# Performance work log

Measured on AMD Instinct MI355X. Metric: run time of the kernel, lower is better.

Reference implementation:

```python
import jax, jax.numpy as jnp
import numpy as np

N, E, D = 50000, 800000, 128

def setup_inputs() -> dict:
    key = jax.random.key(0)
    ks = jax.random.split(key, 8)
    s = 0.02
    x = jax.random.normal(ks[0], (N, D), dtype=jnp.float32)
    edge_index = jax.random.randint(ks[1], (2, E), 0, N, dtype=jnp.int64)
    Wn = jax.random.normal(ks[2], (D, D), dtype=jnp.float32) * s
    bn = jax.random.normal(ks[3], (D,), dtype=jnp.float32) * s
    We = jax.random.normal(ks[4], (D, 2 * D), dtype=jnp.float32) * s
    be = jax.random.normal(ks[5], (D,), dtype=jnp.float32) * s
    Wu = jax.random.normal(ks[6], (D, 3 * D), dtype=jnp.float32) * s
    bu = jax.random.normal(ks[7], (D,), dtype=jnp.float32) * s
    return {"x": x, "edge_index": edge_index, "Wn": Wn, "bn": bn,
            "We": We, "be": be, "Wu": Wu, "bu": bu}

def reference(x, edge_index, Wn, bn, We, be, Wu, bu):
    n = x.shape[0]
    # 1. per-node linear transform (torch Linear: x @ W.T + b)
    node = x @ Wn.T + bn                                   # [N, D]
    src, dst = edge_index[0], edge_index[1]
    # 2. per-edge embedding from concatenated endpoint node embeddings
    edge_in = jnp.concatenate([node[src], node[dst]], axis=1)  # [E, 2D]
    edge_emb = edge_in @ We.T + be                          # [E, D]
    # 3. scatter-sum neighbor node embeddings and incident edge embeddings to src vertex
    nbr_sum = jax.ops.segment_sum(node[dst], src, num_segments=n)    # [N, D]
    edge_sum = jax.ops.segment_sum(edge_emb, src, num_segments=n)   # [N, D]
    pre_gelu = jnp.concatenate([node, nbr_sum, edge_sum], axis=1)    # [N, 3D]
    # 4-5. GELU (exact, matching torch nn.GELU default) + final linear
    out = jax.nn.gelu(pre_gelu, approximate=False) @ Wu.T + bu       # [N, D]
    return out
```

## Files before the change

### kernel.cpp

```cpp
#include <hip/hip_runtime.h>
#include <hip/hip_bf16.h>
#include <math.h>

typedef __attribute__((ext_vector_type(8))) short short8;
typedef __attribute__((ext_vector_type(4))) float f32x4;

#define CAP8 16
#define EPT  8

__device__ __forceinline__ float bf2f(unsigned short u) {
    union { unsigned int i; float f; } c; c.i = ((unsigned int)u) << 16; return c.f;
}
__device__ __forceinline__ unsigned short f2bf(float f) {
    __hip_bfloat16 h = __float2bfloat16(f);
    union { __hip_bfloat16 h; unsigned short u; } c; c.h = h; return c.u;
}
__device__ __forceinline__ float gelu_exact(float x) {
    return 0.5f * x * (1.0f + erff(x * 0.7071067811865475f));
}
__device__ __forceinline__ short8 ldcvt8(const float* p) {
    float4 f0 = *(const float4*)p;
    float4 f1 = *(const float4*)(p + 4);
    short8 a;
    a[0] = (short)f2bf(f0.x); a[1] = (short)f2bf(f0.y);
    a[2] = (short)f2bf(f0.z); a[3] = (short)f2bf(f0.w);
    a[4] = (short)f2bf(f1.x); a[5] = (short)f2bf(f1.y);
    a[6] = (short)f2bf(f1.z); a[7] = (short)f2bf(f1.w);
    return a;
}
__device__ __forceinline__ int swz(int row, int colbyte) {
    return row * 256 + (colbyte ^ ((row & 7) << 4));
}

__device__ __forceinline__ int detect_flag(const int* ei, int E) {
    int orv = 0;
    int lim = (E < 64) ? E : 64;
    for (int i = 0; i < lim; i++) orv |= ei[2 * i + 1];
    return (orv == 0) ? 1 : 0;
}
__device__ __forceinline__ int ld_src(const int* ei, int flag, int E, int e) {
    if (flag) { int2 p = *(const int2*)(ei + 2 * (size_t)e); return p.x; }
    return ei[e];
}
__device__ __forceinline__ int ld_dst(const int* ei, int flag, int E, int e) {
    if (flag) { int2 p = *(const int2*)(ei + 2 * (size_t)(E + e)); return p.x; }
    return ei[E + e];
}

__launch_bounds__(256)
__global__ void init_kernel(const float* __restrict__ Wn, const float* __restrict__ We,
                            const float* __restrict__ Wu,
                            unsigned short* __restrict__ Wnb, unsigned short* __restrict__ Web,
                            unsigned short* __restrict__ Wub,
                            int* __restrict__ cursor8, int N) {
    const int stride = gridDim.x * 256;
    const int t = blockIdx.x * 256 + threadIdx.x;
    for (int i = t; i < 8 * N; i += stride) cursor8[i] = 0;
    for (int i = t; i < 128 * 128; i += stride) Wnb[i] = f2bf(Wn[i]);
    for (int i = t; i < 128 * 256; i += stride) Web[i] = f2bf(We[i]);
    for (int i = t; i < 128 * 384; i += stride) Wub[i] = f2bf(Wu[i]);
}

__device__ __forceinline__ void gemm1_body(int bid,
                                           const float* __restrict__ x,
                                           const unsigned short* __restrict__ Wnb,
                                           const float* __restrict__ bias,
                                           unsigned short* __restrict__ node,
                                           unsigned short* __restrict__ Apre0,
                                           int N) {
    const int v0 = bid * 64;
    const int wave = threadIdx.x >> 6;
    const int lane = threadIdx.x & 63;
    const int m    = lane & 15;
    const int kq   = lane >> 4;

    short8 B[2][4];
#pragma unroll
    for (int ntl = 0; ntl < 2; ntl++) {
        const int j = (wave * 2 + ntl) * 16 + m;
#pragma unroll
        for (int kb = 0; kb < 4; kb++)
            B[ntl][kb] = *(const short8*)(Wnb + (size_t)j * 128 + kb * 32 + kq * 8);
    }

    f32x4 acc[4][2];
#pragma unroll
    for (int mt = 0; mt < 4; mt++)
#pragma unroll
        for (int ntl = 0; ntl < 2; ntl++) acc[mt][ntl] = (f32x4){0.f,0.f,0.f,0.f};

#pragma unroll
    for (int kb = 0; kb < 4; kb++) {
#pragma unroll
        for (int mt = 0; mt < 4; mt++) {
            const int row = v0 + mt * 16 + m;
            short8 a = (short8){0,0,0,0,0,0,0,0};
            if (row < N) a = ldcvt8(x + (size_t)row * 128 + kb * 32 + kq * 8);
#pragma unroll
            for (int ntl = 0; ntl < 2; ntl++)
                acc[mt][ntl] = __builtin_amdgcn_mfma_f32_16x16x32_bf16(a, B[ntl][kb], acc[mt][ntl], 0, 0, 0);
        }
    }

    const int ocol = lane & 15;
#pragma unroll
    for (int mt = 0; mt < 4; mt++) {
#pragma unroll
        for (int ntl = 0; ntl < 2; ntl++) {
            const int col = (wave * 2 + ntl) * 16 + ocol;
            const float bval = bias[col];
#pragma unroll
            for (int r = 0; r < 4; r++) {
                const int row = v0 + mt * 16 + (lane >> 4) * 4 + r;
                if (row < N) {
                    const float v = acc[mt][ntl][r] + bval;
                    node[(size_t)row * 128 + col]  = f2bf(v);
                    Apre0[(size_t)row * 128 + col] = f2bf(gelu_exact(v));
                }
            }
        }
    }
}

__launch_bounds__(256)
__global__ void fused_a(const float* __restrict__ x,
                        const unsigned short* __restrict__ Wnb,
                        const float* __restrict__ bn,
                        unsigned short* __restrict__ node,
                        unsigned short* __restrict__ Apre0,
                        const int* __restrict__ ei,
                        int* __restrict__ cursor8,
                        unsigned short* __restrict__ csr8,
                        int E, int N, int mblocks) {
    const int grp = blockIdx.x >> 3;
    if ((grp % 3) != 0) {
        const int g1 = grp - grp / 3 - 1;
        const int mid = g1 * 8 + (int)(blockIdx.x & 7);
        if (mid < mblocks) gemm1_body(mid, x, Wnb, bn, node, Apre0, N);
        return;
    }
    __shared__ int sflag;
    if (threadIdx.x == 0) sflag = detect_flag(ei, E);
    __syncthreads();
    const int fgrp = grp / 3;
    const int b = (int)(blockIdx.x & 7);
    const int e0 = (fgrp * 8 + b) * (256 * EPT) + (int)threadIdx.x;

    int sv[EPT], dv[EPT], p[EPT];
    bool ok[EPT];
#pragma unroll
    for (int k = 0; k < EPT; k++) {
        const int e = e0 + k * 256;
        ok[k] = (e < E);
        sv[k] = 0; dv[k] = 0; p[k] = CAP8;
        if (ok[k]) { sv[k] = ld_src(ei, sflag, E, e); dv[k] = ld_dst(ei, sflag, E, e); }
    }
#pragma unroll
    for (int k = 0; k < EPT; k++) {
        ok[k] = ok[k] && (unsigned)sv[k] < (unsigned)N && (unsigned)dv[k] < (unsigned)N;
        if (ok[k]) p[k] = atomicAdd(&cursor8[(size_t)b * N + sv[k]], 1);
    }
#pragma unroll
    for (int k = 0; k < EPT; k++) {
        if (ok[k] && p[k] < CAP8)
            csr8[((size_t)b * N + sv[k]) * CAP8 + p[k]] = (unsigned short)dv[k];
    }
}

__launch_bounds__(256)
__global__ void fused_b(const int* __restrict__ cursor8,
                        const unsigned short* __restrict__ csr8,
                        const unsigned short* __restrict__ node,
                        const unsigned short* __restrict__ Apre0,
                        const unsigned short* __restrict__ Web,
                        const float* __restrict__ be,
                        const unsigned short* __restrict__ Wub,
                        const float* __restrict__ bu,
                        float* __restrict__ out, int N) {
    __shared__ unsigned short nbrT [32 * 128];
    __shared__ unsigned short gnbrT[32 * 128];
    __shared__ unsigned short scratch[32 * 128];
    __shared__ int   degBv[32][8];
    __shared__ int   degI[32];
    __shared__ float degF[32];

    const int v0   = blockIdx.x * 32;
    const int tid  = threadIdx.x;
    const int wave = tid >> 6;
    const int lane = tid & 63;
    const int m    = lane & 15;
    const int kq   = lane >> 4;
    const bool full = (v0 + 32 <= N);

    {
        const int vi = tid >> 3, b = tid & 7;
        const int v = v0 + vi;
        int c = (v < N) ? cursor8[(size_t)b * N + v] : 0;
        degBv[vi][b] = (c > CAP8) ? CAP8 : c;
    }
    __syncthreads();
    if (tid < 32) {
        int s = 0;
#pragma unroll
        for (int b = 0; b < 8; b++) s += degBv[tid][b];
        degI[tid] = s; degF[tid] = (float)s;
    }
    __syncthreads();

    {
        unsigned short* listT = scratch;
#pragma unroll
        for (int i = 0; i < 8; i++) {
            const int vl = wave * 8 + i;
            const int v  = v0 + vl;
            if (v >= N) continue;
            const int slot0 = lane, slot1 = lane + 64;
            const unsigned short i0 = csr8[((size_t)(slot0 >> 4) * N + v) * CAP8 + (slot0 & 15)];
            const unsigned short i1 = csr8[((size_t)(slot1 >> 4) * N + v) * CAP8 + (slot1 & 15)];
            const bool vd0 = (slot0 & 15) < degBv[vl][slot0 >> 4];
            const bool vd1 = (slot1 & 15) < degBv[vl][slot1 >> 4];
            const unsigned long long m0 = __ballot(vd0);
            const unsigned long long m1 = __ballot(vd1);
            const unsigned long long below = (1ull << lane) - 1ull;
            const int n0 = __popcll(m0);
            if (vd0) listT[vl * 128 + __popcll(m0 & below)] = i0;
            if (vd1) listT[vl * 128 + n0 + __popcll(m1 & below)] = i1;
        }
        asm volatile("s_waitcnt lgkmcnt(0)" ::: "memory");

        const int way = lane >> 4, sl = lane & 15;
        for (int i = 0; i < 8; i++) {
            const int vl = wave * 8 + i;
            const int v  = v0 + vl;
            if (v >= N) continue;
            const int deg = degI[vl];
            float acc[8] = {0.f,0.f,0.f,0.f,0.f,0.f,0.f,0.f};
            for (int base = 0; base < deg; base += 16) {
                short8 a[4]; int r[4];
#pragma unroll
                for (int u = 0; u < 4; u++) {
                    r[u] = base + way + u * 4;
                    const int id = (r[u] < deg) ? (int)listT[vl * 128 + r[u]] : 0;
                    a[u] = *(const short8*)(node + (size_t)id * 128 + sl * 8);
                }
#pragma unroll
                for (int u = 0; u < 4; u++) {
                    if (r[u] < deg) {
#pragma unroll
                        for (int k = 0; k < 8; k++) acc[k] += bf2f((unsigned short)a[u][k]);
                    }
                }
            }
#pragma unroll
            for (int k = 0; k < 8; k++) {
                acc[k] += __shfl_xor(acc[k], 16);
                acc[k] += __shfl_xor(acc[k], 32);
            }
            if (way == 0) {
                short8 o;
#pragma unroll
                for (int k = 0; k < 8; k++) o[k] = (short)f2bf(acc[k]);
                *(short8*)((char*)nbrT + swz(vl, sl * 16)) = o;
            } else if (way == 1) {
                short8 o;
#pragma unroll
                for (int k = 0; k < 8; k++) o[k] = (short)f2bf(gelu_exact(acc[k]));
                *(short8*)((char*)gnbrT + swz(vl, sl * 16)) = o;
            }
        }
    }
    __syncthreads();

    {
        f32x4 acc2[2][2];
#pragma unroll
        for (int mt = 0; mt < 2; mt++)
#pragma unroll
            for (int ntl = 0; ntl < 2; ntl++) acc2[mt][ntl] = (f32x4){0.f,0.f,0.f,0.f};

#pragma unroll
        for (int kb = 0; kb < 4; kb++) {
            short8 B0[2], B1[2], an[2], ab[2];
#pragma unroll
            for (int ntl = 0; ntl < 2; ntl++) {
                const int j = (wave * 2 + ntl) * 16 + m;
                B0[ntl] = *(const short8*)(Web + (size_t)j * 256 + kb * 32 + kq * 8);
                B1[ntl] = *(const short8*)(Web + (size_t)j * 256 + 128 + kb * 32 + kq * 8);
            }
#pragma unroll
            for (int mt = 0; mt < 2; mt++) {
                const int lrow = mt * 16 + m;
                const int row  = v0 + lrow;
                an[mt] = (full || row < N) ? *(const short8*)(node + (size_t)row * 128 + kb * 32 + kq * 8)
                                           : (short8){0,0,0,0,0,0,0,0};
                ab[mt] = *(const short8*)((const char*)nbrT + swz(lrow, kb * 64 + kq * 16));
            }
#pragma unroll
            for (int mt = 0; mt < 2; mt++) {
                const float dg = degF[mt * 16 + m];
#pragma unroll
                for (int k = 0; k < 8; k++)
                    an[mt][k] = (short)f2bf(dg * bf2f((unsigned short)an[mt][k]));
            }
#pragma unroll
            for (int mt = 0; mt < 2; mt++)
#pragma unroll
                for (int ntl = 0; ntl < 2; ntl++) {
                    acc2[mt][ntl] = __builtin_amdgcn_mfma_f32_16x16x32_bf16(an[mt], B0[ntl], acc2[mt][ntl], 0, 0, 0);
                    acc2[mt][ntl] = __builtin_amdgcn_mfma_f32_16x16x32_bf16(ab[mt], B1[ntl], acc2[mt][ntl], 0, 0, 0);
                }
        }

        const int ocol = lane & 15;
#pragma unroll
        for (int mt = 0; mt < 2; mt++) {
#pragma unroll
            for (int ntl = 0; ntl < 2; ntl++) {
                const int col = (wave * 2 + ntl) * 16 + ocol;
                const float bval = be[col];
#pragma unroll
                for (int r = 0; r < 4; r++) {
                    const int lrow = mt * 16 + (lane >> 4) * 4 + r;
                    const float dg = degF[lrow];
                    const float vv = gelu_exact(acc2[mt][ntl][r] + dg * bval);
                    *(unsigned short*)((char*)scratch + swz(lrow, col * 2)) = f2bf(vv);
                }
            }
        }
    }
    __syncthreads();

    {
        f32x4 acc3[2][2];
#pragma unroll
        for (int mt = 0; mt < 2; mt++)
#pragma unroll
            for (int ntl = 0; ntl < 2; ntl++) acc3[mt][ntl] = (f32x4){0.f,0.f,0.f,0.f};

#pragma unroll
        for (int s = 0; s < 3; s++) {
#pragma unroll
            for (int kb = 0; kb < 4; kb++) {
                short8 B3[2], a[2];
#pragma unroll
                for (int ntl = 0; ntl < 2; ntl++) {
                    const int j = (wave * 2 + ntl) * 16 + m;
                    B3[ntl] = *(const short8*)(Wub + (size_t)j * 384 + s * 128 + kb * 32 + kq * 8);
                }
#pragma unroll
                for (int mt = 0; mt < 2; mt++) {
                    const int lrow = mt * 16 + m;
                    const int row  = v0 + lrow;
                    if (s == 0) {
                        a[mt] = (full || row < N) ? *(const short8*)(Apre0 + (size_t)row * 128 + kb * 32 + kq * 8)
                                                  : (short8){0,0,0,0,0,0,0,0};
                    } else if (s == 1) {
                        a[mt] = *(const short8*)((const char*)gnbrT + swz(lrow, kb * 64 + kq * 16));
                    } else {
                        a[mt] = *(const short8*)((const char*)scratch + swz(lrow, kb * 64 + kq * 16));
                    }
                }
#pragma unroll
                for (int mt = 0; mt < 2; mt++)
#pragma unroll
                    for (int ntl = 0; ntl < 2; ntl++)
                        acc3[mt][ntl] = __builtin_amdgcn_mfma_f32_16x16x32_bf16(a[mt], B3[ntl], acc3[mt][ntl], 0, 0, 0);
            }
        }

        const int ocol = lane & 15;
#pragma unroll
        for (int mt = 0; mt < 2; mt++) {
#pragma unroll
            for (int ntl = 0; ntl < 2; ntl++) {
                const int col = (wave * 2 + ntl) * 16 + ocol;
                const float bval = bu[col];
#pragma unroll
                for (int r = 0; r < 4; r++) {
                    const int row = v0 + mt * 16 + (lane >> 4) * 4 + r;
                    if (row < N)
                        out[(size_t)row * 128 + col] = acc3[mt][ntl][r] + bval;
                }
            }
        }
    }
}

extern "C" void kernel_launch(void* const* d_in, const int* in_sizes, int n_in,
                              void* d_out, int out_size, void* d_ws, size_t ws_size,
                              hipStream_t stream) {
    const float* x  = (const float*)d_in[0];
    const int*   ei = (const int*)d_in[1];
    const float* Wn = (const float*)d_in[2];
    const float* bn = (const float*)d_in[3];
    const float* We = (const float*)d_in[4];
    const float* be = (const float*)d_in[5];
    const float* Wu = (const float*)d_in[6];
    const float* bu = (const float*)d_in[7];

    const int N = in_sizes[0] / 128;
    const int E = in_sizes[1] / 2;

    char* ws = (char*)d_ws;
    size_t off = 0;
    unsigned short* node  = (unsigned short*)(ws + off); off += (size_t)N * 128 * 2;
    unsigned short* Apre0 = (unsigned short*)(ws + off); off += (size_t)N * 128 * 2;
    off = (off + 255) & ~(size_t)255;
    int* cursor8 = (int*)(ws + off);                     off += (size_t)8 * N * 4;
    off = (off + 255) & ~(size_t)255;
    unsigned short* csr8 = (unsigned short*)(ws + off);  off += (size_t)8 * N * CAP8 * 2;
    off = (off + 255) & ~(size_t)255;
    unsigned short* Wnb = (unsigned short*)(ws + off);   off += (size_t)128 * 128 * 2;
    unsigned short* Web = (unsigned short*)(ws + off);   off += (size_t)128 * 256 * 2;
    unsigned short* Wub = (unsigned short*)(ws + off);   off += (size_t)128 * 384 * 2;

    const int mblocks = (N + 63) / 64;
    const int eblocks = (E + 256 * EPT - 1) / (256 * EPT);
    const int fgroups = (eblocks + 7) / 8;
    const int ggroups = (mblocks + 7) / 8;
    const int tgroups = fgroups + ggroups;
    const int grid_a  = tgroups * 8;

    init_kernel<<<512, 256, 0, stream>>>(Wn, We, Wu, Wnb, Web, Wub, cursor8, N);
    fused_a<<<grid_a, 256, 0, stream>>>(x, Wnb, bn, node, Apre0, ei, cursor8, csr8, E, N, mblocks);
    fused_b<<<(N + 31) / 32, 256, 0, stream>>>(cursor8, csr8, node, Apre0, Web, be, Wub, bu, (float*)d_out, N);
}
```

Before: 227.0 us.

## Process neighbor gathers across 8 vertices in node-id chunks for locality

Restructures the neighbor-sum gather so each wave preloads up to 32 packed neighbor ids for all 8 of its vertices. It then sweeps the node table in four id-range chunks, gathering only ids within the current chunk. This aims to improve cache locality across waves and to expose more independent loads per thread than the earlier per-vertex serial loop. The cost is many more predicated checks, higher register pressure from 64 accumulators plus packed ids, and a separate fallback loop for degrees above 32.

```diff
diff --git a/kernel.cpp b/kernel.cpp
--- a/kernel.cpp
+++ b/kernel.cpp
@@ -227,45 +227,84 @@
             if (vd1) listT[vl * 128 + n0 + __popcll(m1 & below)] = i1;
         }
         asm volatile("s_waitcnt lgkmcnt(0)" ::: "memory");
+        __builtin_amdgcn_sched_barrier(0);
 
         const int way = lane >> 4, sl = lane & 15;
+        const int wv8 = wave * 8;
+
+        unsigned pid[8][4];
+#pragma unroll
         for (int i = 0; i < 8; i++) {
-            const int vl = wave * 8 + i;
-            const int v  = v0 + vl;
-            if (v >= N) continue;
-            const int deg = degI[vl];
-            float acc[8] = {0.f,0.f,0.f,0.f,0.f,0.f,0.f,0.f};
-            for (int base = 0; base < deg; base += 16) {
-                short8 a[4]; int r[4];
-#pragma unroll
-                for (int u = 0; u < 4; u++) {
-                    r[u] = base + way + u * 4;
-                    const int id = (r[u] < deg) ? (int)listT[vl * 128 + r[u]] : 0;
-                    a[u] = *(const short8*)(node + (size_t)id * 128 + sl * 8);
-                }
-#pragma unroll
-                for (int u = 0; u < 4; u++) {
-                    if (r[u] < deg) {
-#pragma unroll
-                        for (int k = 0; k < 8; k++) acc[k] += bf2f((unsigned short)a[u][k]);
+            const int vl = wv8 + i;
+            const int dgv = degI[vl];
+#pragma unroll
+            for (int j = 0; j < 4; j++) {
+                const int p0 = way + 8 * j;
+                const int p1 = p0 + 4;
+                const unsigned lo16 = (p0 < dgv) ? (unsigned)listT[vl * 128 + p0] : 0xFFFFu;
+                const unsigned hi16 = (p1 < dgv) ? (unsigned)listT[vl * 128 + p1] : 0xFFFFu;
+                pid[i][j] = lo16 | (hi16 << 16);
+            }
+        }
+
+        float acc[8][8];
+#pragma unroll
+        for (int i = 0; i < 8; i++)
+#pragma unroll
+            for (int e = 0; e < 8; e++) acc[i][e] = 0.f;
+
+        const int CH = (N + 3) >> 2;
+#pragma unroll
+        for (int c = 0; c < 4; c++) {
+            const unsigned lo = (unsigned)(c * CH);
+            const unsigned hi = lo + (unsigned)CH;
+#pragma unroll
+            for (int i = 0; i < 8; i++) {
+#pragma unroll
+                for (int j = 0; j < 4; j++) {
+#pragma unroll
+                    for (int h = 0; h < 2; h++) {
+                        const unsigned id = h ? (pid[i][j] >> 16) : (pid[i][j] & 0xFFFFu);
+                        if (id >= lo && id < hi) {
+                            const short8 t = *(const short8*)(node + (size_t)id * 128 + sl * 8);
+#pragma unroll
+                            for (int e = 0; e < 8; e++) acc[i][e] += bf2f((unsigned short)t[e]);
+                        }
                     }
                 }
             }
-#pragma unroll
-            for (int k = 0; k < 8; k++) {
-                acc[k] += __shfl_xor(acc[k], 16);
-                acc[k] += __shfl_xor(acc[k], 32);
-            }
-            if (way == 0) {
-                short8 o;
-#pragma unroll
-                for (int k = 0; k < 8; k++) o[k] = (short)f2bf(acc[k]);
-                *(short8*)((char*)nbrT + swz(vl, sl * 16)) = o;
-            } else if (way == 1) {
-                short8 o;
-#pragma unroll
-                for (int k = 0; k < 8; k++) o[k] = (short)f2bf(gelu_exact(acc[k]));
-                *(short8*)((char*)gnbrT + swz(vl, sl * 16)) = o;
+        }
+
+#pragma unroll
+        for (int i = 0; i < 8; i++) {
+            const int vl = wv8 + i;
+            const int v_ = v0 + vl;
+            const int dgv = degI[vl];
+            if (__builtin_expect(dgv > 32, 0)) {
+                for (int p = 32 + way; p < dgv; p += 4) {
+                    const int id = (int)listT[vl * 128 + p];
+                    const short8 t = *(const short8*)(node + (size_t)id * 128 + sl * 8);
+#pragma unroll
+                    for (int e = 0; e < 8; e++) acc[i][e] += bf2f((unsigned short)t[e]);
+                }
+            }
+#pragma unroll
+            for (int e = 0; e < 8; e++) {
+                acc[i][e] += __shfl_xor(acc[i][e], 16);
+                acc[i][e] += __shfl_xor(acc[i][e], 32);
+            }
+            if (v_ < N) {
+                if (way == 0) {
+                    short8 o;
+#pragma unroll
+                    for (int e = 0; e < 8; e++) o[e] = (short)f2bf(acc[i][e]);
+                    *(short8*)((char*)nbrT + swz(vl, sl * 16)) = o;
+                } else if (way == 1) {
+                    short8 o;
+#pragma unroll
+                    for (int e = 0; e < 8; e++) o[e] = (short)f2bf(gelu_exact(acc[i][e]));
+                    *(short8*)((char*)gnbrT + swz(vl, sl * 16)) = o;
+                }
             }
         }
     }
```

Result: slower. 542.2 us (+138.9%).
